# Performance work log

Hardware: AMD Instinct MI355X
Metric: run time of the kernel (lower is better)

The kernel has to match this reference:

```python
import jax, jax.numpy as jnp
import numpy as np

TOP_K = 2

def setup_inputs() -> dict:
    key = jax.random.key(0)
    k1, k2, k3, k4 = jax.random.split(key, 4)
    N, H, F, E = 2048, 1024, 2048, 8
    x = jax.random.normal(k1, (N, H), dtype=jnp.float32)
    router_weight = jax.random.normal(k2, (H, E), dtype=jnp.float32) * 0.02
    w1 = jax.random.normal(k3, (E, H, F), dtype=jnp.float32) * 0.02
    w2 = jax.random.normal(k4, (E, F, H), dtype=jnp.float32) * 0.02
    return {"x": x, "router_weight": router_weight, "w1": w1, "w2": w2}

def reference(x, router_weight, w1, w2):
    # Router: softmax over experts, top-k, renormalize (matches torch forward).
    N = x.shape[0]
    E = router_weight.shape[1]
    logits = x.astype(jnp.float32) @ router_weight            # [N, E]
    rprobs = jax.nn.softmax(logits, axis=-1)
    topk_p, topk_i = jax.lax.top_k(rprobs, TOP_K)             # [N, K]
    topk_p = topk_p / jnp.sum(topk_p, axis=-1, keepdims=True)
    # Scatter normalized top-k probs into dense [N, E] gate matrix; zeros
    # everywhere else, so gating subsumes the boolean routing_map.
    probs = jnp.zeros((N, E), dtype=jnp.float32).at[
        jnp.arange(N)[:, None], topk_i].set(topk_p)
    # Expert FFN (same math as permute -> grouped GEMM -> weighted scatter-add:
    # out[t] = sum_e probs[t,e] * gelu(x[t] @ w1[e]) @ w2[e]).
    h = jnp.einsum('nh,ehf->enf', x, w1)                      # [E, N, F]
    h = jax.nn.gelu(h, approximate=False)                     # torch F.gelu is erf-based
    y = jnp.einsum('enf,efh->enh', h, w2)                     # [E, N, H]
    out = jnp.einsum('enh,ne->nh', y, probs.astype(x.dtype))  # weighted combine
    return out
```

## Files before the change

### kernel.cpp

```cpp
#include <hip/hip_runtime.h>
#include <hip/hip_fp16.h>
#include <math.h>

#define NTOK 2048
#define HID  1024
#define FFN  2048
#define NEXP 8

#define BM 128
#define BN 128
#define BK 32
#define MAX_TILES 40
#define TLDA 66

#define WS_COUNTS 0
#define WS_SEG    32
#define WS_PROBS  128
#define WS_LISTS  (128 + NTOK*NEXP*4)
#define WS_XH     262144
#define WS_W1T    (WS_XH + NTOK*HID*2)
#define WS_W2T    (WS_W1T + NEXP*HID*FFN*2)
#define WS_HBUF   (WS_W2T + NEXP*HID*FFN*2)

typedef _Float16 half8 __attribute__((ext_vector_type(8)));
typedef float    f32x4 __attribute__((ext_vector_type(4)));

static __device__ __forceinline__ unsigned short f2h_bits(float f) {
  union { _Float16 h; unsigned short u; } v;
  v.h = (_Float16)f;
  return v.u;
}
static __device__ __forceinline__ unsigned pack2(float a, float b) {
  return (unsigned)f2h_bits(a) | ((unsigned)f2h_bits(b) << 16);
}

#define GLOAD16(gsrc, ldst) \
  __builtin_amdgcn_global_load_lds( \
      (const __attribute__((address_space(1))) unsigned int*)(gsrc), \
      (__attribute__((address_space(3))) unsigned int*)(ldst), 16, 0, 0)

#define VMCNT0 asm volatile("s_waitcnt vmcnt(0)" ::: "memory")

template<int IS_W1>
static __device__ __forceinline__ void transpose4(
    int t0, const float* __restrict__ wsrc, unsigned short* __restrict__ wdst,
    unsigned short (*Ls)[64*TLDA], int tid)
{
  const int row = tid >> 2, cq = tid & 3;
  const int oc  = tid >> 2, rs = tid & 3;
  const int e = t0 >> 9;
  const int R = IS_W1 ? HID : FFN;
  const int C = IS_W1 ? FFN : HID;
  const float* src = wsrc + (size_t)e * HID * FFN;
  unsigned short* dst = wdst + (size_t)e * HID * FFN;
  float4 ld[2][4];

#define TGEOM(tt, r0v, c0v) \
    { const int rem_ = (t0 + (tt)) & 511; \
      r0v = IS_W1 ? ((rem_ >> 5) * 64) : ((rem_ >> 4) * 64); \
      c0v = IS_W1 ? ((rem_ & 31) * 64) : ((rem_ & 15) * 64); }

  {
    int r0, c0; TGEOM(0, r0, c0);
    const float4* sp = reinterpret_cast<const float4*>(
        src + (size_t)(r0 + row) * C + c0 + cq * 16);
#pragma unroll
    for (int j = 0; j < 4; ++j) ld[0][j] = sp[j];
  }
#pragma unroll
  for (int t = 0; t < 4; ++t) {
    if (t < 3) {
      int r0, c0; TGEOM(t + 1, r0, c0);
      const float4* sp = reinterpret_cast<const float4*>(
          src + (size_t)(r0 + row) * C + c0 + cq * 16);
#pragma unroll
      for (int j = 0; j < 4; ++j) ld[(t + 1) & 1][j] = sp[j];
    }
    {
      unsigned* Ld = reinterpret_cast<unsigned*>(Ls[t & 1]);
      const int dbase = row * (TLDA / 2) + cq * 8;
      const float4 a = ld[t & 1][0], b = ld[t & 1][1];
      const float4 c2 = ld[t & 1][2], d = ld[t & 1][3];
      Ld[dbase + 0] = pack2(a.x, a.y);  Ld[dbase + 1] = pack2(a.z, a.w);
      Ld[dbase + 2] = pack2(b.x, b.y);  Ld[dbase + 3] = pack2(b.z, b.w);
      Ld[dbase + 4] = pack2(c2.x, c2.y); Ld[dbase + 5] = pack2(c2.z, c2.w);
      Ld[dbase + 6] = pack2(d.x, d.y);  Ld[dbase + 7] = pack2(d.z, d.w);
    }
    __syncthreads();
    {
      int r0, c0; TGEOM(t, r0, c0);
      unsigned v[8];
#pragma unroll
      for (int j = 0; j < 8; ++j) {
        unsigned lo = Ls[t & 1][(rs * 16 + 2 * j    ) * TLDA + oc];
        unsigned hi = Ls[t & 1][(rs * 16 + 2 * j + 1) * TLDA + oc];
        v[j] = lo | (hi << 16);
      }
      unsigned short* dp = dst + (size_t)(c0 + oc) * R + r0 + rs * 16;
      *reinterpret_cast<uint4*>(dp)     = (uint4){v[0], v[1], v[2], v[3]};
      *reinterpret_cast<uint4*>(dp + 8) = (uint4){v[4], v[5], v[6], v[7]};
    }
  }
#undef TGEOM
}

__global__ __launch_bounds__(256) void moe_prep1(
    const float* __restrict__ x, const float* __restrict__ rw,
    const float* __restrict__ w1,
    unsigned short* __restrict__ xh, unsigned short* __restrict__ w1t,
    int* __restrict__ counts, int* __restrict__ lists, float* __restrict__ probs)
{
  __shared__ unsigned short Ls[2][64 * TLDA];
  const int bid = blockIdx.x;
  const int tid = threadIdx.x;

  if (bid < 1024) {
    transpose4<1>(bid * 4, w1, w1t, Ls, tid);
    return;
  }
  const int wid = tid >> 6, lane = tid & 63;
  const int t = (bid - 1024) * 4 + wid;
  const float* xr = x + (size_t)t * HID + lane * 16;
  const float4* xp = reinterpret_cast<const float4*>(xr);
  float4 v0 = xp[0], v1 = xp[1], v2 = xp[2], v3 = xp[3];
  float xv[16] = {v0.x,v0.y,v0.z,v0.w, v1.x,v1.y,v1.z,v1.w,
                  v2.x,v2.y,v2.z,v2.w, v3.x,v3.y,v3.z,v3.w};
  float acc[NEXP];
#pragma unroll
  for (int e = 0; e < NEXP; ++e) acc[e] = 0.f;
#pragma unroll
  for (int j = 0; j < 16; ++j) {
    const float4* rp = reinterpret_cast<const float4*>(rw + (size_t)(lane*16 + j) * NEXP);
    float4 a = rp[0], b = rp[1];
    acc[0] += xv[j]*a.x; acc[1] += xv[j]*a.y; acc[2] += xv[j]*a.z; acc[3] += xv[j]*a.w;
    acc[4] += xv[j]*b.x; acc[5] += xv[j]*b.y; acc[6] += xv[j]*b.z; acc[7] += xv[j]*b.w;
  }
#pragma unroll
  for (int off = 32; off > 0; off >>= 1) {
#pragma unroll
    for (int e = 0; e < NEXP; ++e) acc[e] += __shfl_down(acc[e], off);
  }
  unsigned short* xd = xh + (size_t)t * HID + lane * 16;
  *reinterpret_cast<uint4*>(xd) =
      (uint4){pack2(v0.x,v0.y), pack2(v0.z,v0.w), pack2(v1.x,v1.y), pack2(v1.z,v1.w)};
  *reinterpret_cast<uint4*>(xd + 8) =
      (uint4){pack2(v2.x,v2.y), pack2(v2.z,v2.w), pack2(v3.x,v3.y), pack2(v3.z,v3.w)};
  if (lane == 0) {
    float m = acc[0];
#pragma unroll
    for (int e = 1; e < NEXP; ++e) m = fmaxf(m, acc[e]);
    float p[NEXP];
#pragma unroll
    for (int e = 0; e < NEXP; ++e) p[e] = expf(acc[e] - m);
    int i0 = 0;
#pragma unroll
    for (int e = 1; e < NEXP; ++e) if (p[e] > p[i0]) i0 = e;
    int i1 = -1;
#pragma unroll
    for (int e = 0; e < NEXP; ++e) {
      if (e == i0) continue;
      if (i1 < 0 || p[e] > p[i1]) i1 = e;
    }
    const float inv = 1.f / (p[i0] + p[i1]);
    probs[t * NEXP + i0] = p[i0] * inv;
    probs[t * NEXP + i1] = p[i1] * inv;
    int pos0 = atomicAdd(&counts[i0], 1); lists[i0 * NTOK + pos0] = t;
    int pos1 = atomicAdd(&counts[i1], 1); lists[i1 * NTOK + pos1] = t;
  }
}

__global__ void moe_segoff(const int* __restrict__ counts, int* __restrict__ seg) {
  if (threadIdx.x == 0 && blockIdx.x == 0) {
    int run = 0;
    for (int e = 0; e < NEXP; ++e) {
      seg[e] = run;
      run += ((counts[e] + BM - 1) / BM) * BM;
    }
    seg[NEXP] = run;
  }
}

__global__ __launch_bounds__(256) void moe_k2(
    const unsigned short* __restrict__ xh, const unsigned short* __restrict__ w1t,
    const float* __restrict__ w2, unsigned short* __restrict__ w2t,
    const int* __restrict__ counts, const int* __restrict__ seg,
    const int* __restrict__ lists, unsigned short* __restrict__ hbuf)
{
  __shared__ __align__(16) unsigned short SMEM[4 * BM * BK];
  __shared__ int tokL[BM];
  const int bid = blockIdx.x;
  const int tid = threadIdx.x;

  if (bid >= MAX_TILES * 16) {
    transpose4<0>((bid - MAX_TILES * 16) * 4, w2, w2t,
                  reinterpret_cast<unsigned short(*)[64 * TLDA]>(SMEM), tid);
    return;
  }

  const int tile = bid >> 4;
  const int jcol = bid & 15;
  const int rb = tile * BM;
  if (rb >= seg[NEXP]) return;
  int e = 0;
#pragma unroll
  for (int q = 1; q < NEXP; ++q) if (seg[q] <= rb) e = q;
  const int cnt = counts[e];
  const int rloc0 = rb - seg[e];

  unsigned short (*Asm)[BM*BK] = reinterpret_cast<unsigned short(*)[BM*BK]>(SMEM);
  unsigned short (*Bsm)[BM*BK] = reinterpret_cast<unsigned short(*)[BM*BK]>(SMEM + 2*BM*BK);

  if (tid < BM) {
    int rl = rloc0 + tid;
    tokL[tid] = (rl < cnt) ? lists[e * NTOK + rl] : 0;
  }
  __syncthreads();

  const int lane = tid & 63;
  const int wid = tid >> 6;
  const int wr = (wid >> 1) * 64;
  const int wc = (wid & 1) * 64;
  const int lr = (lane >> 4) * 4;
  const int lc = lane & 15;
  const int khi = (lane >> 4) * 8;

  const int cw8 = (lane & 3) * 8;
  const int r0 = wid*16 + (lane >> 2);
  const unsigned short* abase[2];
  const unsigned short* bbase[2];
  abase[0] = xh + (size_t)tokL[r0]      * HID + cw8;
  abase[1] = xh + (size_t)tokL[64 + r0] * HID + cw8;
  bbase[0] = w1t + ((size_t)e * FFN + jcol*BN + r0)      * HID + cw8;
  bbase[1] = w1t + ((size_t)e * FFN + jcol*BN + 64 + r0) * HID + cw8;

  f32x4 acc[4][4];
#pragma unroll
  for (int m = 0; m < 4; ++m)
#pragma unroll
    for (int n = 0; n < 4; ++n)
      acc[m][n] = (f32x4){0.f, 0.f, 0.f, 0.f};

#define STAGE1(buf, kk) do { \
    _Pragma("unroll") \
    for (int i = 0; i < 2; ++i) { \
      GLOAD16(abase[i] + (kk), &Asm[buf][(i*256 + wid*64)*8]); \
      GLOAD16(bbase[i] + (kk), &Bsm[buf][(i*256 + wid*64)*8]); \
    } } while (0)

  STAGE1(0, 0);
  VMCNT0;
  __syncthreads();
  int cur = 0;
  for (int kk = 0; kk < HID; kk += BK) {
    if (kk + BK < HID) STAGE1(cur ^ 1, kk + BK);
    half8 af[4], bf[4];
#pragma unroll
    for (int m = 0; m < 4; ++m)
      af[m] = *reinterpret_cast<const half8*>(&Asm[cur][(wr + m*16 + lc)*BK + khi]);
#pragma unroll
    for (int n = 0; n < 4; ++n)
      bf[n] = *reinterpret_cast<const half8*>(&Bsm[cur][(wc + n*16 + lc)*BK + khi]);
#pragma unroll
    for (int m = 0; m < 4; ++m)
#pragma unroll
      for (int n = 0; n < 4; ++n)
        acc[m][n] = __builtin_amdgcn_mfma_f32_16x16x32_f16(af[m], bf[n], acc[m][n], 0, 0, 0);
    VMCNT0;
    __syncthreads();
    cur ^= 1;
  }
#undef STAGE1

#pragma unroll
  for (int m = 0; m < 4; ++m) {
#pragma unroll
    for (int r = 0; r < 4; ++r) {
      unsigned short* hp = hbuf + (size_t)(rb + wr + m*16 + lr + r) * FFN + jcol*BN + wc + lc;
#pragma unroll
      for (int n = 0; n < 4; ++n) {
        float v = acc[m][n][r];
        float g = 0.5f * v * (1.f + erff(v * 0.70710678118f));
        hp[n*16] = f2h_bits(g);
      }
    }
  }
}

__global__ __launch_bounds__(256) void moe_gemm2(
    const unsigned short* __restrict__ hbuf, const unsigned short* __restrict__ w2t,
    const int* __restrict__ counts, const int* __restrict__ seg,
    const int* __restrict__ lists, const float* __restrict__ probs,
    float* __restrict__ out)
{
  const int tile = blockIdx.x >> 4;
  const int jcol = (blockIdx.x >> 1) & 7;
  const int ks   = blockIdx.x & 1;
  const int rb = tile * BM;
  if (rb >= seg[NEXP]) return;
  int e = 0;
#pragma unroll
  for (int q = 1; q < NEXP; ++q) if (seg[q] <= rb) e = q;
  const int cnt = counts[e];
  const int rloc0 = rb - seg[e];
  const int k0 = ks * (FFN / 2);
  const int k1 = k0 + (FFN / 2);

  __shared__ int tokL[BM];
  __shared__ float pL[BM];
  __shared__ __align__(16) unsigned short Asm[2][BM*BK];
  __shared__ __align__(16) unsigned short Bsm[2][BM*BK];

  const int tid = threadIdx.x;
  if (tid < BM) {
    int rl = rloc0 + tid;
    if (rl < cnt) {
      int tk = lists[e * NTOK + rl];
      tokL[tid] = tk;
      pL[tid] = probs[tk * NEXP + e];
    } else { tokL[tid] = 0; pL[tid] = 0.f; }
  }
  __syncthreads();

  const int lane = tid & 63;
  const int wid = tid >> 6;
  const int wr = (wid >> 1) * 64;
  const int wc = (wid & 1) * 64;
  const int lr = (lane >> 4) * 4;
  const int lc = lane & 15;
  const int khi = (lane >> 4) * 8;

  const int cw8 = (lane & 3) * 8;
  const int r0 = wid*16 + (lane >> 2);
  const unsigned short* abase[2];
  const unsigned short* bbase[2];
  abase[0] = hbuf + (size_t)(rb + r0)      * FFN + cw8;
  abase[1] = hbuf + (size_t)(rb + 64 + r0) * FFN + cw8;
  bbase[0] = w2t + ((size_t)e * HID + jcol*BN + r0)      * FFN + cw8;
  bbase[1] = w2t + ((size_t)e * HID + jcol*BN + 64 + r0) * FFN + cw8;

  f32x4 acc[4][4];
#pragma unroll
  for (int m = 0; m < 4; ++m)
#pragma unroll
    for (int n = 0; n < 4; ++n)
      acc[m][n] = (f32x4){0.f, 0.f, 0.f, 0.f};

#define STAGE2(buf, kk) do { \
    _Pragma("unroll") \
    for (int i = 0; i < 2; ++i) { \
      GLOAD16(abase[i] + (kk), &Asm[buf][(i*256 + wid*64)*8]); \
      GLOAD16(bbase[i] + (kk), &Bsm[buf][(i*256 + wid*64)*8]); \
    } } while (0)

  STAGE2(0, k0);
  VMCNT0;
  __syncthreads();
  int cur = 0;
  for (int kk = k0; kk < k1; kk += BK) {
    if (kk + BK < k1) STAGE2(cur ^ 1, kk + BK);
    half8 af[4], bf[4];
#pragma unroll
    for (int m = 0; m < 4; ++m)
      af[m] = *reinterpret_cast<const half8*>(&Asm[cur][(wr + m*16 + lc)*BK + khi]);
#pragma unroll
    for (int n = 0; n < 4; ++n)
      bf[n] = *reinterpret_cast<const half8*>(&Bsm[cur][(wc + n*16 + lc)*BK + khi]);
#pragma unroll
    for (int m = 0; m < 4; ++m)
#pragma unroll
      for (int n = 0; n < 4; ++n)
        acc[m][n] = __builtin_amdgcn_mfma_f32_16x16x32_f16(af[m], bf[n], acc[m][n], 0, 0, 0);
    VMCNT0;
    __syncthreads();
    cur ^= 1;
  }
#undef STAGE2

#pragma unroll
  for (int m = 0; m < 4; ++m) {
#pragma unroll
    for (int r = 0; r < 4; ++r) {
      const int lrow = wr + m*16 + lr + r;
      const int rl = rloc0 + lrow;
      if (rl >= cnt) continue;
      const int tok = tokL[lrow];
      const float p = pL[lrow];
      float* op = out + (size_t)tok * HID + jcol*BN + wc + lc;
#pragma unroll
      for (int n = 0; n < 4; ++n)
        atomicAdd(&op[n*16], p * acc[m][n][r]);
    }
  }
}

extern "C" void kernel_launch(void* const* d_in, const int* in_sizes, int n_in,
                              void* d_out, int out_size, void* d_ws, size_t ws_size,
                              hipStream_t stream) {
  const float* x  = (const float*)d_in[0];
  const float* rw = (const float*)d_in[1];
  const float* w1 = (const float*)d_in[2];
  const float* w2 = (const float*)d_in[3];
  float* out = (float*)d_out;

  char* ws = (char*)d_ws;
  int*   counts = (int*)(ws + WS_COUNTS);
  int*   seg    = (int*)(ws + WS_SEG);
  float* probs  = (float*)(ws + WS_PROBS);
  int*   lists  = (int*)(ws + WS_LISTS);
  unsigned short* xh   = (unsigned short*)(ws + WS_XH);
  unsigned short* w1t  = (unsigned short*)(ws + WS_W1T);
  unsigned short* w2t  = (unsigned short*)(ws + WS_W2T);
  unsigned short* hbuf = (unsigned short*)(ws + WS_HBUF);

  hipMemsetAsync(ws, 0, 128, stream);
  hipMemsetAsync(d_out, 0, (size_t)NTOK * HID * sizeof(float), stream);

  moe_prep1<<<1024 + NTOK/4, 256, 0, stream>>>(x, rw, w1, xh, w1t,
                                               counts, lists, probs);
  moe_segoff<<<1, 64, 0, stream>>>(counts, seg);
  moe_k2<<<MAX_TILES * 16 + 1024, 256, 0, stream>>>(xh, w1t, w2, w2t,
                                                    counts, seg, lists, hbuf);
  moe_gemm2<<<MAX_TILES * (HID / BN) * 2, 256, 0, stream>>>(hbuf, w2t, counts, seg, lists, probs, out);
}
```

Before: 184.6 us.

## Fuse w1 fp32-to-fp16 conversion into GEMM1 B-tile loading, drop w1 transpose pass

Removes the separate pass that transposed and converted w1 to fp16 in the prep kernel. GEMM1 now reads fp32 w1 directly into registers, converts with packed cvt_pkrtz and writes a padded LDS tile, software-pipelined with the next load. This avoids writing and re-reading a 32MB fp16 copy, but every tile re-reads fp32 w1 (twice the bytes per tile across many row tiles) and does conversion work in the GEMM loop.

```diff
diff --git a/kernel.cpp b/kernel.cpp
--- a/kernel.cpp
+++ b/kernel.cpp
@@ -10,6 +10,7 @@
 #define BM 128
 #define BN 128
 #define BK 32
+#define LDK 36
 #define MAX_TILES 40
 #define TLDA 66
 
@@ -18,12 +19,13 @@
 #define WS_PROBS  128
 #define WS_LISTS  (128 + NTOK*NEXP*4)
 #define WS_XH     262144
-#define WS_W1T    (WS_XH + NTOK*HID*2)
-#define WS_W2T    (WS_W1T + NEXP*HID*FFN*2)
-#define WS_HBUF   (WS_W2T + NEXP*HID*FFN*2)
+#define WS_W2T    (WS_XH + NTOK*HID*2)
+#define WS_HBUF   (WS_W2T + (size_t)NEXP*HID*FFN*2)
 
 typedef _Float16 half8 __attribute__((ext_vector_type(8)));
+typedef __fp16   fp16x2 __attribute__((ext_vector_type(2)));
 typedef float    f32x4 __attribute__((ext_vector_type(4)));
+typedef unsigned long long u64;
 
 static __device__ __forceinline__ unsigned short f2h_bits(float f) {
   union { _Float16 h; unsigned short u; } v;
@@ -31,7 +33,14 @@
   return v.u;
 }
 static __device__ __forceinline__ unsigned pack2(float a, float b) {
-  return (unsigned)f2h_bits(a) | ((unsigned)f2h_bits(b) << 16);
+  union { fp16x2 h; unsigned u; } v;
+  v.h[0] = (__fp16)a; v.h[1] = (__fp16)b;
+  return v.u;
+}
+static __device__ __forceinline__ unsigned cvt2(float a, float b) {
+  union { fp16x2 h; unsigned u; } t;
+  t.h = __builtin_amdgcn_cvt_pkrtz(a, b);
+  return t.u;
 }
 
 #define GLOAD16(gsrc, ldst) \
@@ -104,22 +113,15 @@
 #undef TGEOM
 }
 
-__global__ __launch_bounds__(256) void moe_prep1(
+__global__ __launch_bounds__(256) void moe_prep(
     const float* __restrict__ x, const float* __restrict__ rw,
-    const float* __restrict__ w1,
-    unsigned short* __restrict__ xh, unsigned short* __restrict__ w1t,
+    unsigned short* __restrict__ xh,
     int* __restrict__ counts, int* __restrict__ lists, float* __restrict__ probs)
 {
-  __shared__ unsigned short Ls[2][64 * TLDA];
-  const int bid = blockIdx.x;
   const int tid = threadIdx.x;
-
-  if (bid < 1024) {
-    transpose4<1>(bid * 4, w1, w1t, Ls, tid);
-    return;
-  }
   const int wid = tid >> 6, lane = tid & 63;
-  const int t = (bid - 1024) * 4 + wid;
+  const int t = blockIdx.x * 4 + wid;
+
   const float* xr = x + (size_t)t * HID + lane * 16;
   const float4* xp = reinterpret_cast<const float4*>(xr);
   float4 v0 = xp[0], v1 = xp[1], v2 = xp[2], v3 = xp[3];
@@ -181,12 +183,12 @@
 }
 
 __global__ __launch_bounds__(256) void moe_k2(
-    const unsigned short* __restrict__ xh, const unsigned short* __restrict__ w1t,
+    const unsigned short* __restrict__ xh, const float* __restrict__ w1,
     const float* __restrict__ w2, unsigned short* __restrict__ w2t,
     const int* __restrict__ counts, const int* __restrict__ seg,
     const int* __restrict__ lists, unsigned short* __restrict__ hbuf)
 {
-  __shared__ __align__(16) unsigned short SMEM[4 * BM * BK];
+  __shared__ __align__(16) unsigned short SMEM[2*BM*BK + 2*128*LDK];
   __shared__ int tokL[BM];
   const int bid = blockIdx.x;
   const int tid = threadIdx.x;
@@ -207,8 +209,8 @@
   const int cnt = counts[e];
   const int rloc0 = rb - seg[e];
 
-  unsigned short (*Asm)[BM*BK] = reinterpret_cast<unsigned short(*)[BM*BK]>(SMEM);
-  unsigned short (*Bsm)[BM*BK] = reinterpret_cast<unsigned short(*)[BM*BK]>(SMEM + 2*BM*BK);
+  unsigned short (*Asm)[BM*BK]   = reinterpret_cast<unsigned short(*)[BM*BK]>(SMEM);
+  unsigned short (*Bsm)[128*LDK] = reinterpret_cast<unsigned short(*)[128*LDK]>(SMEM + 2*BM*BK);
 
   if (tid < BM) {
     int rl = rloc0 + tid;
@@ -227,11 +229,12 @@
   const int cw8 = (lane & 3) * 8;
   const int r0 = wid*16 + (lane >> 2);
   const unsigned short* abase[2];
-  const unsigned short* bbase[2];
   abase[0] = xh + (size_t)tokL[r0]      * HID + cw8;
   abase[1] = xh + (size_t)tokL[64 + r0] * HID + cw8;
-  bbase[0] = w1t + ((size_t)e * FFN + jcol*BN + r0)      * HID + cw8;
-  bbase[1] = w1t + ((size_t)e * FFN + jcol*BN + 64 + r0) * HID + cw8;
+
+  const int kb = tid >> 5;
+  const int fb = tid & 31;
+  const float* bbase = w1 + (size_t)e * HID * FFN + (size_t)jcol * 128 + fb * 4;
 
   f32x4 acc[4][4];
 #pragma unroll
@@ -240,42 +243,67 @@
     for (int n = 0; n < 4; ++n)
       acc[m][n] = (f32x4){0.f, 0.f, 0.f, 0.f};
 
-#define STAGE1(buf, kk) do { \
+  f32x4 bld[4];
+
+#define LOADB1(kk) do { \
     _Pragma("unroll") \
-    for (int i = 0; i < 2; ++i) { \
-      GLOAD16(abase[i] + (kk), &Asm[buf][(i*256 + wid*64)*8]); \
-      GLOAD16(bbase[i] + (kk), &Bsm[buf][(i*256 + wid*64)*8]); \
+    for (int j = 0; j < 4; ++j) \
+      bld[j] = *reinterpret_cast<const f32x4*>(bbase + (size_t)((kk) + kb*4 + j) * FFN); \
+  } while (0)
+
+#define STAGEA1(buf, kk) do { \
+    GLOAD16(abase[0] + (kk), &Asm[buf][(wid*64)*8]); \
+    GLOAD16(abase[1] + (kk), &Asm[buf][(256 + wid*64)*8]); \
+  } while (0)
+
+#define CVTB1(buf) do { \
+    _Pragma("unroll") \
+    for (int i3 = 0; i3 < 4; ++i3) { \
+      uint2 wv; \
+      wv.x = cvt2(bld[0][i3], bld[1][i3]); \
+      wv.y = cvt2(bld[2][i3], bld[3][i3]); \
+      *reinterpret_cast<uint2*>(&Bsm[buf][(fb*4 + i3)*LDK + kb*4]) = wv; \
     } } while (0)
 
-  STAGE1(0, 0);
-  VMCNT0;
-  __syncthreads();
+  LOADB1(0);
+  STAGEA1(0, 0);
   int cur = 0;
   for (int kk = 0; kk < HID; kk += BK) {
-    if (kk + BK < HID) STAGE1(cur ^ 1, kk + BK);
+    CVTB1(cur);
+    VMCNT0;
+    __syncthreads();
+    if (kk + BK < HID) {
+      LOADB1(kk + BK);
+      STAGEA1(cur ^ 1, kk + BK);
+    }
     half8 af[4], bf[4];
 #pragma unroll
     for (int m = 0; m < 4; ++m)
       af[m] = *reinterpret_cast<const half8*>(&Asm[cur][(wr + m*16 + lc)*BK + khi]);
 #pragma unroll
-    for (int n = 0; n < 4; ++n)
-      bf[n] = *reinterpret_cast<const half8*>(&Bsm[cur][(wc + n*16 + lc)*BK + khi]);
+    for (int n = 0; n < 4; ++n) {
+      union { u64 q[2]; half8 h; } t;
+      const unsigned short* bp = &Bsm[cur][(wc + n*16 + lc)*LDK + khi];
+      t.q[0] = *reinterpret_cast<const u64*>(bp);
+      t.q[1] = *reinterpret_cast<const u64*>(bp + 4);
+      bf[n] = t.h;
+    }
 #pragma unroll
     for (int m = 0; m < 4; ++m)
 #pragma unroll
       for (int n = 0; n < 4; ++n)
         acc[m][n] = __builtin_amdgcn_mfma_f32_16x16x32_f16(af[m], bf[n], acc[m][n], 0, 0, 0);
-    VMCNT0;
-    __syncthreads();
     cur ^= 1;
   }
-#undef STAGE1
+#undef LOADB1
+#undef STAGEA1
+#undef CVTB1
 
 #pragma unroll
   for (int m = 0; m < 4; ++m) {
 #pragma unroll
     for (int r = 0; r < 4; ++r) {
-      unsigned short* hp = hbuf + (size_t)(rb + wr + m*16 + lr + r) * FFN + jcol*BN + wc + lc;
+      unsigned short* hp = hbuf + (size_t)(rb + wr + m*16 + lr + r) * FFN + jcol*128 + wc + lc;
 #pragma unroll
       for (int n = 0; n < 4; ++n) {
         float v = acc[m][n][r];
@@ -408,17 +436,15 @@
   float* probs  = (float*)(ws + WS_PROBS);
   int*   lists  = (int*)(ws + WS_LISTS);
   unsigned short* xh   = (unsigned short*)(ws + WS_XH);
-  unsigned short* w1t  = (unsigned short*)(ws + WS_W1T);
   unsigned short* w2t  = (unsigned short*)(ws + WS_W2T);
   unsigned short* hbuf = (unsigned short*)(ws + WS_HBUF);
 
   hipMemsetAsync(ws, 0, 128, stream);
   hipMemsetAsync(d_out, 0, (size_t)NTOK * HID * sizeof(float), stream);
 
-  moe_prep1<<<1024 + NTOK/4, 256, 0, stream>>>(x, rw, w1, xh, w1t,
-                                               counts, lists, probs);
+  moe_prep<<<NTOK/4, 256, 0, stream>>>(x, rw, xh, counts, lists, probs);
   moe_segoff<<<1, 64, 0, stream>>>(counts, seg);
-  moe_k2<<<MAX_TILES * 16 + 1024, 256, 0, stream>>>(xh, w1t, w2, w2t,
+  moe_k2<<<MAX_TILES * 16 + 1024, 256, 0, stream>>>(xh, w1, w2, w2t,
                                                     counts, seg, lists, hbuf);
-  moe_gemm2<<<MAX_TILES * (HID / BN) * 2, 256, 0, stream>>>(hbuf, w2t, counts, seg, lists, probs, out);
-}
+  moe_gemm2<<<MAX_TILES * 8 * 2, 256, 0, stream>>>(hbuf, w2t, counts, seg, lists, probs, out);
+}
```

Result: faster. 175.9 us (median of 3 runs) (-4.7%).
